# Optimization experiments

Hardware: AMD Instinct MI355X
Metric: run time of the kernel (lower is better)

The kernel has to match this reference:

```python
import jax, jax.numpy as jnp
import numpy as np

NUM_GROUPS = 32
EPS = 1e-6
HEAD = 8


def group_norm(x, gamma, beta):
    # x: (b, c, h, w); normalize per group of channels over (c/g, h, w)
    b, c, h, w = x.shape
    g = NUM_GROUPS
    xg = x.reshape(b, g, c // g, h, w)
    mean = xg.mean(axis=(2, 3, 4), keepdims=True)
    var = xg.var(axis=(2, 3, 4), keepdims=True)
    xn = ((xg - mean) * jax.lax.rsqrt(var + EPS)).reshape(b, c, h, w)
    return xn * gamma[None, :, None, None] + beta[None, :, None, None]


def setup_inputs() -> dict:
    key = jax.random.key(0)
    ks = jax.random.split(key, 6)
    b, c, h, w = 8, 512, 64, 64
    sd = 1.0 / np.sqrt(c)
    return {
        "x": jax.random.normal(ks[0], (b, c, h, w), jnp.float32),
        "gamma": jnp.ones((c,), jnp.float32),
        "beta": jnp.zeros((c,), jnp.float32),
        "Wq": jax.random.normal(ks[1], (c, c), jnp.float32) * sd,
        "Wk": jax.random.normal(ks[2], (c, c), jnp.float32) * sd,
        "Wv": jax.random.normal(ks[3], (c, c), jnp.float32) * sd,
        "Wp": jax.random.normal(ks[4], (c, c), jnp.float32) * sd,
        "bp": jnp.zeros((c,), jnp.float32),
    }


def reference(x, gamma, beta, Wq, Wk, Wv, Wp, bp):
    b, c, h, w = x.shape
    hd = c // HEAD
    scale = jnp.sqrt(jnp.float32(hd))  # NOTE: original MULTIPLIES by sqrt(d)
    xn = group_norm(x, gamma, beta)            # (b, c, h, w)
    x_ = xn.reshape(b, c, h * w).transpose(0, 2, 1)  # (b, n, c), n = h*w
    # torch Linear: y = x @ W.T
    Q = (x_ @ Wq.T).reshape(b, h * w, HEAD, hd)
    K = (x_ @ Wk.T).reshape(b, h * w, HEAD, hd)
    V = (x_ @ Wv.T).reshape(b, h * w, HEAD, hd)
    # einsum 'bhid,bhjd->bhij' with axes (b, n, head, hd): per-position head gram
    dots = jnp.einsum('bnid,bnjd->bnij', Q, K) * scale  # (b, n, head, head)
    att = jax.nn.softmax(dots, axis=1)  # softmax over the SPATIAL axis (dim=1)
    out = jnp.einsum('bnij,bnjd->bnid', att, V).reshape(b, h * w, c)
    out = out @ Wp.T + bp  # dropout is identity at inference
    return out.transpose(0, 2, 1).reshape(b, c, h, w) + xn  # residual adds normed x
```

## Files before the change

kernel.cpp:

```cpp
#include <hip/hip_runtime.h>
#include <stdint.h>

typedef unsigned short ushort_t;
typedef _Float16 half8 __attribute__((ext_vector_type(8)));
typedef float f32x4 __attribute__((ext_vector_type(4)));

#define GLOBAL_AS __attribute__((address_space(1)))
#define LDS_AS    __attribute__((address_space(3)))

__device__ __forceinline__ float bf2f(ushort_t u) {
    union { unsigned i; float f; } v; v.i = ((unsigned)u) << 16; return v.f;
}
__device__ __forceinline__ ushort_t f2h(float f) {
    union { _Float16 h; ushort_t u; } v; v.h = (_Float16)f; return v.u;
}
__device__ __forceinline__ float h2f(ushort_t u) {
    union { _Float16 h; ushort_t u; } v; v.u = u; return (float)v.h;
}

__device__ __forceinline__ void async16(const void* g, void* l) {
    __builtin_amdgcn_global_load_lds((const GLOBAL_AS uint32_t*)g,
                                     (LDS_AS uint32_t*)l, 16, 0, 0);
}

__device__ __forceinline__ int is_bf16_in(const uint32_t* g32) {
    return *g32 == 0x3F803F80u;
}

__global__ __launch_bounds__(256) void vecconv(const void* g, const void* be, const void* bp,
                                               float* gcan, float* bcan, float* bpcan,
                                               const uint32_t* g32) {
    int t = threadIdx.x + blockIdx.x * 256;
    if (is_bf16_in(g32)) {
        gcan[t]  = bf2f(((const ushort_t*)g)[t]);
        bcan[t]  = bf2f(((const ushort_t*)be)[t]);
        bpcan[t] = bf2f(((const ushort_t*)bp)[t]);
    } else {
        gcan[t]  = ((const float*)g)[t];
        bcan[t]  = ((const float*)be)[t];
        bpcan[t] = ((const float*)bp)[t];
    }
}

__global__ __launch_bounds__(256) void wconv(const void* Wq, const void* Wk,
                                             const void* Wv, const void* Wp,
                                             ushort_t* Wh, const uint32_t* g32) {
    const void* src = (blockIdx.y == 0) ? Wq : (blockIdx.y == 1) ? Wk
                    : (blockIdx.y == 2) ? Wv : Wp;
    ushort_t* dst = Wh + (size_t)blockIdx.y * 262144;
    const int e0 = blockIdx.x * 2048 + threadIdx.x * 8;
    ushort_t o[8];
    if (is_bf16_in(g32)) {
        uint4 u = *(const uint4*)((const ushort_t*)src + e0);
        const ushort_t* e = (const ushort_t*)&u;
#pragma unroll
        for (int j = 0; j < 8; ++j) o[j] = f2h(bf2f(e[j]));
    } else {
        float4 a = *(const float4*)((const float*)src + e0);
        float4 b = *(const float4*)((const float*)src + e0 + 4);
        o[0] = f2h(a.x); o[1] = f2h(a.y); o[2] = f2h(a.z); o[3] = f2h(a.w);
        o[4] = f2h(b.x); o[5] = f2h(b.y); o[6] = f2h(b.z); o[7] = f2h(b.w);
    }
    *(uint4*)(dst + e0) = *(const uint4*)o;
}

__global__ __launch_bounds__(256) void gn_part(const void* xv, float* __restrict__ psums,
                                               const uint32_t* g32) {
    const int bx = blockIdx.x, t = threadIdx.x;
    const size_t base = (size_t)(bx >> 3) * 65536 + (size_t)(bx & 7) * 8192;
    float s = 0.f, sq = 0.f;
    if (is_bf16_in(g32)) {
        const ushort_t* p = (const ushort_t*)xv + base;
        for (int i = 0; i < 4; ++i) {
            uint4 u = ((const uint4*)p)[t + 256 * i];
            const ushort_t* e = (const ushort_t*)&u;
#pragma unroll
            for (int j = 0; j < 8; ++j) { float f = bf2f(e[j]); s += f; sq += f * f; }
        }
    } else {
        const float* p = (const float*)xv + base;
        for (int i = 0; i < 8; ++i) {
            float4 v = ((const float4*)p)[t + 256 * i];
            s += v.x + v.y + v.z + v.w;
            sq += v.x * v.x + v.y * v.y + v.z * v.z + v.w * v.w;
        }
    }
    __shared__ float ls[256], lq[256];
    ls[t] = s; lq[t] = sq;
    __syncthreads();
    for (int off = 128; off > 0; off >>= 1) {
        if (t < off) { ls[t] += ls[t + off]; lq[t] += lq[t + off]; }
        __syncthreads();
    }
    if (t == 0) { psums[bx * 2] = ls[0]; psums[bx * 2 + 1] = lq[0]; }
}

__global__ __launch_bounds__(256) void gn_fin(const float* __restrict__ psums,
                                              float* __restrict__ stats) {
    const int t = threadIdx.x;
    float s = 0.f, q = 0.f;
#pragma unroll
    for (int k = 0; k < 8; ++k) { s += psums[(t * 8 + k) * 2]; q += psums[(t * 8 + k) * 2 + 1]; }
    float mean = s * (1.f / 65536.f);
    float var  = q * (1.f / 65536.f) - mean * mean;
    stats[t * 2 + 0] = mean;
    stats[t * 2 + 1] = rsqrtf(fmaxf(var, 0.f) + 1e-6f);
}

__global__ __launch_bounds__(256) void gn_apply_t(const void* xv,
                                                  const float* __restrict__ gcan,
                                                  const float* __restrict__ bcan,
                                                  const float* __restrict__ stats,
                                                  ushort_t* __restrict__ xnt,
                                                  ushort_t* __restrict__ xnc,
                                                  const uint32_t* g32) {
    const int nt = blockIdx.x;
    const int ct = blockIdx.y;
    const int b  = blockIdx.z;
    const int t  = threadIdx.x;
    const int c0 = ct * 64, n0 = nt * 64;
    __shared__ __align__(16) ushort_t tile[64 * 80];
    if (is_bf16_in(g32)) {
        const ushort_t* x = (const ushort_t*)xv;
#pragma unroll
        for (int p = 0; p < 2; ++p) {
            int u = p * 256 + t;
            int cc = u >> 3, nc = u & 7;
            int c = c0 + cc;
            size_t gidx = ((size_t)(b * 512 + c)) * 4096 + n0 + nc * 8;
            uint4 raw = *(const uint4*)(x + gidx);
            float mean = stats[(b * 32 + (c >> 4)) * 2 + 0];
            float rstd = stats[(b * 32 + (c >> 4)) * 2 + 1];
            float sc = rstd * gcan[c];
            float sh = bcan[c] - mean * sc;
            const ushort_t* e = (const ushort_t*)&raw;
            ushort_t hv[8];
#pragma unroll
            for (int j = 0; j < 8; ++j) {
                hv[j] = f2h(bf2f(e[j]) * sc + sh);
                tile[(nc * 8 + j) * 80 + cc] = hv[j];
            }
            *(uint4*)(xnc + gidx) = *(const uint4*)hv;
        }
    } else {
        const float* x = (const float*)xv;
#pragma unroll
        for (int p = 0; p < 4; ++p) {
            int u = p * 256 + t;
            int cc = u >> 4, nc = u & 15;
            int c = c0 + cc;
            size_t gidx = ((size_t)(b * 512 + c)) * 4096 + n0 + nc * 4;
            float4 raw = *(const float4*)(x + gidx);
            float mean = stats[(b * 32 + (c >> 4)) * 2 + 0];
            float rstd = stats[(b * 32 + (c >> 4)) * 2 + 1];
            float sc = rstd * gcan[c];
            float sh = bcan[c] - mean * sc;
            ushort_t hv[4];
            hv[0] = f2h(raw.x * sc + sh);
            hv[1] = f2h(raw.y * sc + sh);
            hv[2] = f2h(raw.z * sc + sh);
            hv[3] = f2h(raw.w * sc + sh);
#pragma unroll
            for (int j = 0; j < 4; ++j) tile[(nc * 4 + j) * 80 + cc] = hv[j];
            *(uint2*)(xnc + gidx) = *(const uint2*)hv;
        }
    }
    __syncthreads();
#pragma unroll
    for (int p = 0; p < 2; ++p) {
        int u = p * 256 + t;
        int nn = u >> 3, cchunk = u & 7;
        uint4 o = *(const uint4*)(tile + nn * 80 + cchunk * 8);
        *(uint4*)(xnt + ((size_t)(b * 4096 + n0 + nn)) * 512 + c0 + cchunk * 8) = o;
    }
}

__device__ __forceinline__ void gemm128_core(const ushort_t* __restrict__ A,
                                             const ushort_t* __restrict__ B,
                                             int m0, int n0, int K, f32x4 acc[4][4]) {
    __shared__ __align__(16) ushort_t As[128 * 32];
    __shared__ __align__(16) ushort_t Bs[128 * 32];
    const int t = threadIdx.x;
    const int l = t & 63;
    const int w = t >> 6;
    const int wm = (w >> 1) * 64, wn = (w & 1) * 64;
    const int lr = l & 15, q = l >> 4;
    f32x4 zero = {0.f, 0.f, 0.f, 0.f};
#pragma unroll
    for (int mi = 0; mi < 4; ++mi)
#pragma unroll
        for (int ni = 0; ni < 4; ++ni) acc[mi][ni] = zero;

    for (int kt = 0; kt < K; kt += 32) {
        __syncthreads();
#pragma unroll
        for (int p = 0; p < 2; ++p) {
            int s = p * 256 + t;
            int r = s >> 2, kc = s & 3;
            async16(A + (size_t)(m0 + r) * K + kt + kc * 8, (char*)As + p * 4096 + w * 1024);
            async16(B + (size_t)(n0 + r) * K + kt + kc * 8, (char*)Bs + p * 4096 + w * 1024);
        }
        __syncthreads();
        half8 af[4], bf[4];
#pragma unroll
        for (int mi = 0; mi < 4; ++mi)
            af[mi] = *(const half8*)(As + (wm + mi * 16 + lr) * 32 + q * 8);
#pragma unroll
        for (int ni = 0; ni < 4; ++ni)
            bf[ni] = *(const half8*)(Bs + (wn + ni * 16 + lr) * 32 + q * 8);
#pragma unroll
        for (int mi = 0; mi < 4; ++mi)
#pragma unroll
            for (int ni = 0; ni < 4; ++ni)
                acc[mi][ni] = __builtin_amdgcn_mfma_f32_16x16x32_f16(af[mi], bf[ni],
                                                                    acc[mi][ni], 0, 0, 0);
    }
}

__global__ __launch_bounds__(256) void gemm_qkv(const ushort_t* __restrict__ xnt,
                                                const ushort_t* __restrict__ Wh,
                                                ushort_t* __restrict__ Qo,
                                                ushort_t* __restrict__ Ko,
                                                ushort_t* __restrict__ Vo) {
    const int id = blockIdx.x;
    const int xcd = id & 7, s = id >> 3;
    const int mloc = s / 12, r = s % 12;
    const int m0 = (xcd * 32 + mloc) * 128;
    const int n0 = (r & 3) * 128;
    const int z  = r >> 2;
    const ushort_t* B = Wh + (size_t)z * 262144;
    ushort_t* C = (z == 0) ? Qo : (z == 1) ? Ko : Vo;
    f32x4 acc[4][4];
    gemm128_core(xnt, B, m0, n0, 512, acc);
    const int t = threadIdx.x, l = t & 63, w = t >> 6;
    const int wm = (w >> 1) * 64, wn = (w & 1) * 64;
    const int col = l & 15, q = l >> 4;
#pragma unroll
    for (int mi = 0; mi < 4; ++mi)
#pragma unroll
        for (int ni = 0; ni < 4; ++ni)
#pragma unroll
            for (int rr = 0; rr < 4; ++rr) {
                int row = wm + mi * 16 + q * 4 + rr;
                int cc  = wn + ni * 16 + col;
                C[(size_t)(m0 + row) * 512 + n0 + cc] = f2h(acc[mi][ni][rr]);
            }
}

__global__ __launch_bounds__(256) void dots_k(const ushort_t* __restrict__ Q,
                                              const ushort_t* __restrict__ K,
                                              float* __restrict__ dots) {
    const int t = threadIdx.x, l = t & 63, w = t >> 6;
    const int gp0 = blockIdx.x * 8 + w * 2;
    const int m = l & 15, q = l >> 4;
    const size_t base = (size_t)(gp0 + (m >> 3)) * 512 + (m & 7) * 64 + q * 8;
    half8 a0 = *(const half8*)(Q + base);
    half8 a1 = *(const half8*)(Q + base + 32);
    half8 b0 = *(const half8*)(K + base);
    half8 b1 = *(const half8*)(K + base + 32);
    f32x4 acc = {0.f, 0.f, 0.f, 0.f};
    acc = __builtin_amdgcn_mfma_f32_16x16x32_f16(a0, b0, acc, 0, 0, 0);
    acc = __builtin_amdgcn_mfma_f32_16x16x32_f16(a1, b1, acc, 0, 0, 0);
    const int col = l & 15;
#pragma unroll
    for (int r = 0; r < 4; ++r) {
        int row = q * 4 + r;
        if (row < 8 && col < 8)
            dots[(size_t)gp0 * 64 + row * 8 + col] = acc[r] * 8.0f;
        if (row >= 8 && col >= 8)
            dots[(size_t)(gp0 + 1) * 64 + (row - 8) * 8 + (col - 8)] = acc[r] * 8.0f;
    }
}

__global__ __launch_bounds__(256) void smax_part(const float* __restrict__ dots,
                                                 float* __restrict__ pmax,
                                                 float* __restrict__ psum) {
    const int chunk = blockIdx.x;
    const int t = threadIdx.x;
    const int ij = t & 63, sub = t >> 6;
    const size_t base = ((size_t)chunk * 128 + sub * 32) * 64 + ij;
    float v[32];
    float m = -1e30f;
#pragma unroll
    for (int r = 0; r < 32; ++r) { v[r] = dots[base + (size_t)r * 64]; m = fmaxf(m, v[r]); }
    __shared__ float lm[4][64];
    __shared__ float lsum[4][64];
    lm[sub][ij] = m;
    __syncthreads();
    float cm = fmaxf(fmaxf(lm[0][ij], lm[1][ij]), fmaxf(lm[2][ij], lm[3][ij]));
    float s = 0.f;
#pragma unroll
    for (int r = 0; r < 32; ++r) s += __expf(v[r] - cm);
    lsum[sub][ij] = s;
    __syncthreads();
    if (sub == 0) {
        pmax[chunk * 64 + ij] = cm;
        psum[chunk * 64 + ij] = lsum[0][ij] + lsum[1][ij] + lsum[2][ij] + lsum[3][ij];
    }
}

__global__ __launch_bounds__(64) void smax_final(const float* __restrict__ pmax,
                                                 const float* __restrict__ psum,
                                                 float* __restrict__ Mout,
                                                 float* __restrict__ Sinv) {
    const int b = blockIdx.x;
    const int ij = threadIdx.x;
    float pm[32];
    float M = -1e30f;
#pragma unroll
    for (int c = 0; c < 32; ++c) { pm[c] = pmax[(b * 32 + c) * 64 + ij]; M = fmaxf(M, pm[c]); }
    float S = 0.f;
#pragma unroll
    for (int c = 0; c < 32; ++c) S += psum[(b * 32 + c) * 64 + ij] * __expf(pm[c] - M);
    Mout[b * 64 + ij] = M;
    Sinv[b * 64 + ij] = 1.f / S;
}

__global__ __launch_bounds__(256) void attn_apply(const float* __restrict__ dots,
                                                  const float* __restrict__ Mbuf,
                                                  const float* __restrict__ Sinv,
                                                  const ushort_t* __restrict__ V,
                                                  ushort_t* __restrict__ P) {
    const int t = threadIdx.x, l = t & 63, w = t >> 6;
    const int gp = blockIdx.x * 4 + w;
    const int b = gp >> 12;
    __shared__ float att[4][64];
    __shared__ __align__(16) ushort_t vb[4][512];
    float d = dots[(size_t)gp * 64 + l];
    att[w][l] = __expf(d - Mbuf[b * 64 + l]) * Sinv[b * 64 + l];
    *(uint4*)(&vb[w][l * 8]) = *(const uint4*)(V + (size_t)gp * 512 + l * 8);
    __syncthreads();
    const int i = l >> 3, dc = l & 7;
    float o[8] = {0, 0, 0, 0, 0, 0, 0, 0};
#pragma unroll
    for (int j = 0; j < 8; ++j) {
        float a = att[w][i * 8 + j];
        uint4 vv = *(const uint4*)(&vb[w][j * 64 + dc * 8]);
        const ushort_t* ve = (const ushort_t*)&vv;
#pragma unroll
        for (int k2 = 0; k2 < 8; ++k2) o[k2] += a * h2f(ve[k2]);
    }
    ushort_t ou[8];
#pragma unroll
    for (int k2 = 0; k2 < 8; ++k2) ou[k2] = f2h(o[k2]);
    *(uint4*)(P + (size_t)gp * 512 + l * 8) = *(const uint4*)ou;
}

__global__ __launch_bounds__(256) void gemm_out(const ushort_t* __restrict__ Wph,
                                                const ushort_t* __restrict__ P,
                                                const ushort_t* __restrict__ xnc,
                                                const float* __restrict__ bpcan,
                                                float* __restrict__ out) {
    const int id = blockIdx.x;
    const int xcd = id & 7, s = id >> 3;
    const int pair = xcd * 32 + (s >> 2);
    const int o0 = (s & 3) * 128;
    const int b  = pair >> 5;
    const int n0 = (pair & 31) * 128;
    f32x4 acc[4][4];
    gemm128_core(Wph, P + (size_t)b * 4096 * 512, o0, n0, 512, acc);
    const int t = threadIdx.x, l = t & 63, w = t >> 6;
    const int wm = (w >> 1) * 64, wn = (w & 1) * 64;
    const int col = l & 15, q = l >> 4;
#pragma unroll
    for (int mi = 0; mi < 4; ++mi) {
#pragma unroll
        for (int r = 0; r < 4; ++r) {
            int o = o0 + wm + mi * 16 + q * 4 + r;
            float bias = bpcan[o];
#pragma unroll
            for (int ni = 0; ni < 4; ++ni) {
                int n = n0 + wn + ni * 16 + col;
                size_t idx = ((size_t)(b * 512 + o)) * 4096 + n;
                out[idx] = acc[mi][ni][r] + bias + h2f(xnc[idx]);
            }
        }
    }
}

extern "C" void kernel_launch(void* const* d_in, const int* in_sizes, int n_in,
                              void* d_out, int out_size, void* d_ws, size_t ws_size,
                              hipStream_t stream) {
    const void* x     = d_in[0];
    const void* gamma = d_in[1];
    const void* beta  = d_in[2];
    const void* Wq    = d_in[3];
    const void* Wk    = d_in[4];
    const void* Wv    = d_in[5];
    const void* Wp    = d_in[6];
    const void* bp    = d_in[7];
    const uint32_t* g32 = (const uint32_t*)gamma;
    float* out = (float*)d_out;

    char* ws = (char*)d_ws;
    const size_t SZ = 33554432;
    ushort_t* xnt = (ushort_t*)(ws);
    ushort_t* Qh  = (ushort_t*)(ws + 1 * SZ);
    ushort_t* Kh  = (ushort_t*)(ws + 2 * SZ);
    ushort_t* Vh  = (ushort_t*)(ws + 3 * SZ);
    float* dots   = (float*)(ws + 4 * SZ);
    ushort_t* Wh  = (ushort_t*)(ws + 4 * SZ + 8388608);
    ushort_t* xnc = (ushort_t*)(ws + 4 * SZ + 8388608 + 2097152);
    char* tail    = ws + 4 * SZ + 8388608 + 2097152 + SZ;
    float* gcan   = (float*)(tail);
    float* bcan   = gcan + 512;
    float* bpcan  = bcan + 512;
    float* stats  = bpcan + 512;
    float* psums  = stats + 512;
    float* pmax   = psums + 4096;
    float* psumS  = pmax + 16384;
    float* Mbuf   = psumS + 16384;
    float* Sinv   = Mbuf + 512;
    ushort_t* Pb  = xnt;

    vecconv   <<<2, 256, 0, stream>>>(gamma, beta, bp, gcan, bcan, bpcan, g32);
    wconv     <<<dim3(128, 4), 256, 0, stream>>>(Wq, Wk, Wv, Wp, Wh, g32);
    gn_part   <<<2048, 256, 0, stream>>>(x, psums, g32);
    gn_fin    <<<1, 256, 0, stream>>>(psums, stats);
    gn_apply_t<<<dim3(64, 8, 8), 256, 0, stream>>>(x, gcan, bcan, stats, xnt, xnc, g32);
    gemm_qkv  <<<3072, 256, 0, stream>>>(xnt, Wh, Qh, Kh, Vh);
    dots_k    <<<4096, 256, 0, stream>>>(Qh, Kh, dots);
    smax_part <<<256, 256, 0, stream>>>(dots, pmax, psumS);
    smax_final<<<8, 64, 0, stream>>>(pmax, psumS, Mbuf, Sinv);
    attn_apply<<<8192, 256, 0, stream>>>(dots, Mbuf, Sinv, Vh, Pb);
    gemm_out  <<<1024, 256, 0, stream>>>(Wh + 3 * 262144, Pb, xnc, bpcan, out);
}
```

Measured before the change: 294.2 us.

## Fuse dots and partial softmax kernels; deepen GEMM K-tile with XOR-swizzled LDS

The per-position head-gram kernel and the partial softmax reduction are merged into one kernel. Each block computes 128 positions' 8x8 dot matrices into LDS and reduces max/sum from there, so the dots buffer is no longer re-read from global memory and one launch disappears. The shared GEMM core now loads K-tiles of 64 instead of 32, halving loop iterations and barriers, with an XOR swizzle on the LDS chunks to avoid bank conflicts. The fused kernel launches only 256 blocks, which may limit parallelism, and the larger LDS tiles raise per-block LDS use.

```diff
diff --git a/kernel.cpp b/kernel.cpp
--- a/kernel.cpp
+++ b/kernel.cpp
@@ -178,8 +178,8 @@
 __device__ __forceinline__ void gemm128_core(const ushort_t* __restrict__ A,
                                              const ushort_t* __restrict__ B,
                                              int m0, int n0, int K, f32x4 acc[4][4]) {
-    __shared__ __align__(16) ushort_t As[128 * 32];
-    __shared__ __align__(16) ushort_t Bs[128 * 32];
+    __shared__ __align__(16) ushort_t As[128 * 64];
+    __shared__ __align__(16) ushort_t Bs[128 * 64];
     const int t = threadIdx.x;
     const int l = t & 63;
     const int w = t >> 6;
@@ -191,29 +191,39 @@
 #pragma unroll
         for (int ni = 0; ni < 4; ++ni) acc[mi][ni] = zero;
 
-    for (int kt = 0; kt < K; kt += 32) {
+    for (int kt = 0; kt < K; kt += 64) {
         __syncthreads();
 #pragma unroll
-        for (int p = 0; p < 2; ++p) {
+        for (int p = 0; p < 4; ++p) {
             int s = p * 256 + t;
-            int r = s >> 2, kc = s & 3;
-            async16(A + (size_t)(m0 + r) * K + kt + kc * 8, (char*)As + p * 4096 + w * 1024);
-            async16(B + (size_t)(n0 + r) * K + kt + kc * 8, (char*)Bs + p * 4096 + w * 1024);
+            int r = s >> 3, c = s & 7;
+            int gc = c ^ (r & 7);
+            async16(A + (size_t)(m0 + r) * K + kt + gc * 8, (char*)As + p * 4096 + w * 1024);
+            async16(B + (size_t)(n0 + r) * K + kt + gc * 8, (char*)Bs + p * 4096 + w * 1024);
         }
         __syncthreads();
-        half8 af[4], bf[4];
-#pragma unroll
-        for (int mi = 0; mi < 4; ++mi)
-            af[mi] = *(const half8*)(As + (wm + mi * 16 + lr) * 32 + q * 8);
-#pragma unroll
-        for (int ni = 0; ni < 4; ++ni)
-            bf[ni] = *(const half8*)(Bs + (wn + ni * 16 + lr) * 32 + q * 8);
-#pragma unroll
-        for (int mi = 0; mi < 4; ++mi)
-#pragma unroll
-            for (int ni = 0; ni < 4; ++ni)
-                acc[mi][ni] = __builtin_amdgcn_mfma_f32_16x16x32_f16(af[mi], bf[ni],
-                                                                    acc[mi][ni], 0, 0, 0);
+#pragma unroll
+        for (int h = 0; h < 2; ++h) {
+            half8 af[4], bf[4];
+#pragma unroll
+            for (int mi = 0; mi < 4; ++mi) {
+                int row = wm + mi * 16 + lr;
+                int ch = (h * 4 + q) ^ (lr & 7);
+                af[mi] = *(const half8*)(As + row * 64 + ch * 8);
+            }
+#pragma unroll
+            for (int ni = 0; ni < 4; ++ni) {
+                int row = wn + ni * 16 + lr;
+                int ch = (h * 4 + q) ^ (lr & 7);
+                bf[ni] = *(const half8*)(Bs + row * 64 + ch * 8);
+            }
+#pragma unroll
+            for (int mi = 0; mi < 4; ++mi)
+#pragma unroll
+                for (int ni = 0; ni < 4; ++ni)
+                    acc[mi][ni] = __builtin_amdgcn_mfma_f32_16x16x32_f16(af[mi], bf[ni],
+                                                                        acc[mi][ni], 0, 0, 0);
+        }
     }
 }
 
@@ -247,53 +257,60 @@
             }
 }
 
-__global__ __launch_bounds__(256) void dots_k(const ushort_t* __restrict__ Q,
-                                              const ushort_t* __restrict__ K,
-                                              float* __restrict__ dots) {
-    const int t = threadIdx.x, l = t & 63, w = t >> 6;
-    const int gp0 = blockIdx.x * 8 + w * 2;
-    const int m = l & 15, q = l >> 4;
-    const size_t base = (size_t)(gp0 + (m >> 3)) * 512 + (m & 7) * 64 + q * 8;
-    half8 a0 = *(const half8*)(Q + base);
-    half8 a1 = *(const half8*)(Q + base + 32);
-    half8 b0 = *(const half8*)(K + base);
-    half8 b1 = *(const half8*)(K + base + 32);
-    f32x4 acc = {0.f, 0.f, 0.f, 0.f};
-    acc = __builtin_amdgcn_mfma_f32_16x16x32_f16(a0, b0, acc, 0, 0, 0);
-    acc = __builtin_amdgcn_mfma_f32_16x16x32_f16(a1, b1, acc, 0, 0, 0);
-    const int col = l & 15;
-#pragma unroll
-    for (int r = 0; r < 4; ++r) {
-        int row = q * 4 + r;
-        if (row < 8 && col < 8)
-            dots[(size_t)gp0 * 64 + row * 8 + col] = acc[r] * 8.0f;
-        if (row >= 8 && col >= 8)
-            dots[(size_t)(gp0 + 1) * 64 + (row - 8) * 8 + (col - 8)] = acc[r] * 8.0f;
-    }
-}
-
-__global__ __launch_bounds__(256) void smax_part(const float* __restrict__ dots,
+__global__ __launch_bounds__(256) void dots_smax(const ushort_t* __restrict__ Q,
+                                                 const ushort_t* __restrict__ K,
+                                                 float* __restrict__ dots,
                                                  float* __restrict__ pmax,
                                                  float* __restrict__ psum) {
     const int chunk = blockIdx.x;
-    const int t = threadIdx.x;
-    const int ij = t & 63, sub = t >> 6;
-    const size_t base = ((size_t)chunk * 128 + sub * 32) * 64 + ij;
+    const int t = threadIdx.x, l = t & 63, w = t >> 6;
+    const int m = l & 15, q = l >> 4, col = m;
+    __shared__ float sd[128][64];
+    __shared__ float lm[4][64], lsum[4][64];
+#pragma unroll
+    for (int i = 0; i < 16; ++i) {
+        int gpl = (i * 4 + w) * 2;
+        int gp0 = chunk * 128 + gpl;
+        const size_t base = (size_t)(gp0 + (m >> 3)) * 512 + (m & 7) * 64 + q * 8;
+        half8 a0 = *(const half8*)(Q + base);
+        half8 a1 = *(const half8*)(Q + base + 32);
+        half8 b0 = *(const half8*)(K + base);
+        half8 b1 = *(const half8*)(K + base + 32);
+        f32x4 acc = {0.f, 0.f, 0.f, 0.f};
+        acc = __builtin_amdgcn_mfma_f32_16x16x32_f16(a0, b0, acc, 0, 0, 0);
+        acc = __builtin_amdgcn_mfma_f32_16x16x32_f16(a1, b1, acc, 0, 0, 0);
+#pragma unroll
+        for (int r = 0; r < 4; ++r) {
+            int row = q * 4 + r;
+            if (row < 8 && col < 8) {
+                float v = acc[r] * 8.0f;
+                int ij = row * 8 + col;
+                sd[gpl][ij] = v;
+                dots[(size_t)(gp0)*64 + ij] = v;
+            }
+            if (row >= 8 && col >= 8) {
+                float v = acc[r] * 8.0f;
+                int ij = (row - 8) * 8 + (col - 8);
+                sd[gpl + 1][ij] = v;
+                dots[(size_t)(gp0 + 1) * 64 + ij] = v;
+            }
+        }
+    }
+    __syncthreads();
+    const int ij = l;
+    float mx = -1e30f;
     float v[32];
-    float m = -1e30f;
-#pragma unroll
-    for (int r = 0; r < 32; ++r) { v[r] = dots[base + (size_t)r * 64]; m = fmaxf(m, v[r]); }
-    __shared__ float lm[4][64];
-    __shared__ float lsum[4][64];
-    lm[sub][ij] = m;
+#pragma unroll
+    for (int r = 0; r < 32; ++r) { v[r] = sd[w * 32 + r][ij]; mx = fmaxf(mx, v[r]); }
+    lm[w][ij] = mx;
     __syncthreads();
     float cm = fmaxf(fmaxf(lm[0][ij], lm[1][ij]), fmaxf(lm[2][ij], lm[3][ij]));
-    float s = 0.f;
-#pragma unroll
-    for (int r = 0; r < 32; ++r) s += __expf(v[r] - cm);
-    lsum[sub][ij] = s;
-    __syncthreads();
-    if (sub == 0) {
+    float sum = 0.f;
+#pragma unroll
+    for (int r = 0; r < 32; ++r) sum += __expf(v[r] - cm);
+    lsum[w][ij] = sum;
+    __syncthreads();
+    if (w == 0) {
         pmax[chunk * 64 + ij] = cm;
         psum[chunk * 64 + ij] = lsum[0][ij] + lsum[1][ij] + lsum[2][ij] + lsum[3][ij];
     }
@@ -419,8 +436,7 @@
     gn_fin    <<<1, 256, 0, stream>>>(psums, stats);
     gn_apply_t<<<dim3(64, 8, 8), 256, 0, stream>>>(x, gcan, bcan, stats, xnt, xnc, g32);
     gemm_qkv  <<<3072, 256, 0, stream>>>(xnt, Wh, Qh, Kh, Vh);
-    dots_k    <<<4096, 256, 0, stream>>>(Qh, Kh, dots);
-    smax_part <<<256, 256, 0, stream>>>(dots, pmax, psumS);
+    dots_smax <<<256, 256, 0, stream>>>(Qh, Kh, dots, pmax, psumS);
     smax_final<<<8, 64, 0, stream>>>(pmax, psumS, Mbuf, Sinv);
     attn_apply<<<8192, 256, 0, stream>>>(dots, Mbuf, Sinv, Vh, Pb);
     gemm_out  <<<1024, 256, 0, stream>>>(Wh + 3 * 262144, Pb, xnc, bpcan, out);
```

Result: no change. 292.5 us (-0.6%).
